# Optimization experiments

Measured on AMD Instinct MI355X. Metric: run time of the kernel, lower is better.

Reference implementation:

```python
import jax, jax.numpy as jnp
import numpy as np

J = 1.0          # coupling constant
PT_PERIOD = 4    # parallel-tempering exchange every PT_PERIOD sweeps


def setup_inputs() -> dict:
    key = jax.random.key(0)
    k1, k2 = jax.random.split(key)
    B, C, L = 32, 16, 256
    # temperatures across the Ising critical region, sorted ascending
    T = jnp.sort(1.5 + 2.0 * jax.random.uniform(k1, (B,), dtype=jnp.float32))
    # spins stored as {0,1} ints; converted to +/-1 inside reference
    spins = jax.random.randint(k2, (B, C, L, L), 0, 2).astype(jnp.int32)
    return {"T": T, "spins": spins, "n_sweeps": 16}


def _neighbor_sum(s):
    # periodic 4-neighbor sum, shape preserved [B,C,L,L]
    return (jnp.roll(s, 1, -1) + jnp.roll(s, -1, -1)
            + jnp.roll(s, 1, -2) + jnp.roll(s, -1, -2))


def _energy(s):
    # total Ising energy per chain: -J * sum_<ij> s_i s_j  -> [B, C]
    return -J * jnp.sum(s * (jnp.roll(s, -1, -1) + jnp.roll(s, -1, -2)), axis=(-1, -2))


def reference(T, spins, n_sweeps):
    B, C, L, _ = spins.shape
    s = spins.astype(jnp.float32) * 2.0 - 1.0          # +/-1 spins
    ii = jnp.arange(L)
    parity = (ii[:, None] + ii[None, :]) % 2            # [L,L] checkerboard
    Tb = T[:, None, None, None]                         # [B,1,1,1]
    beta = 1.0 / T                                      # [B]
    base_key = jax.random.key(42)

    def half_sweep(s, key, color):
        dE = 2.0 * J * s * _neighbor_sum(s)             # local energy change on flip
        u = jax.random.uniform(key, s.shape, dtype=jnp.float32)
        acc = u < jnp.exp(-dE / Tb)                     # Metropolis accept
        mask = (parity == color)                        # update one sub-lattice only
        return jnp.where(mask & acc, -s, s)

    def pt_swap(s, key, pair_parity):
        # attempt swaps between adjacent temperatures (b, b+1) with given pair parity
        E = _energy(s)                                  # [B, C]
        d = (beta[:-1] - beta[1:])[:, None] * (E[:-1] - E[1:])   # [B-1, C]
        u = jax.random.uniform(key, (B - 1, C), dtype=jnp.float32)
        pair_mask = (jnp.arange(B - 1) % 2) == pair_parity
        acc = (u < jnp.exp(d)) & pair_mask[:, None]     # [B-1, C] non-overlapping
        swap_next = jnp.concatenate([acc, jnp.zeros((1, C), bool)], 0)  # swap b<->b+1
        swap_prev = jnp.concatenate([jnp.zeros((1, C), bool), acc], 0)
        s_next = jnp.roll(s, -1, axis=0)
        s_prev = jnp.roll(s, 1, axis=0)
        swn = swap_next[:, :, None, None]
        swp = swap_prev[:, :, None, None]
        return jnp.where(swn, s_next, jnp.where(swp, s_prev, s))

    def sweep(s, t):
        kb = jax.random.fold_in(base_key, t)
        k1, k2, k3 = jax.random.split(kb, 3)
        s = half_sweep(s, k1, 0)   # black sub-lattice
        s = half_sweep(s, k2, 1)   # white sub-lattice
        do_pt = (t % PT_PERIOD) == (PT_PERIOD - 1)
        s = jax.lax.cond(do_pt,
                         lambda s_: pt_swap(s_, k3, (t // PT_PERIOD) % 2),
                         lambda s_: s_, s)
        return s, None

    s, _ = jax.lax.scan(sweep, s, jnp.arange(n_sweeps))
    return s, _energy(s)
```

## Files before the change

kernel.cpp:

```cpp
#include <hip/hip_runtime.h>
#include <stdint.h>


#define BB 32
#define CC 16
#define PLANE 65536
#define NSITE (BB * CC * PLANE)
#define NPAIR ((BB - 1) * CC)

__host__ __device__ __forceinline__ void tf2x32(uint32_t k0, uint32_t k1,
                                                uint32_t c0, uint32_t c1,
                                                uint32_t& o0, uint32_t& o1) {
  uint32_t ks2 = k0 ^ k1 ^ 0x1BD11BDAu;
  uint32_t x0 = c0 + k0;
  uint32_t x1 = c1 + k1;
#define TF_ROT(r) { x0 += x1; x1 = (x1 << (r)) | (x1 >> (32 - (r))); x1 ^= x0; }
  TF_ROT(13) TF_ROT(15) TF_ROT(26) TF_ROT(6)
  x0 += k1;  x1 += ks2 + 1u;
  TF_ROT(17) TF_ROT(29) TF_ROT(16) TF_ROT(24)
  x0 += ks2; x1 += k0 + 2u;
  TF_ROT(13) TF_ROT(15) TF_ROT(26) TF_ROT(6)
  x0 += k0;  x1 += k1 + 3u;
  TF_ROT(17) TF_ROT(29) TF_ROT(16) TF_ROT(24)
  x0 += k1;  x1 += ks2 + 4u;
  TF_ROT(13) TF_ROT(15) TF_ROT(26) TF_ROT(6)
  x0 += ks2; x1 += k0 + 5u;
#undef TF_ROT
  o0 = x0; o1 = x1;
}

__device__ __forceinline__ uint32_t rotl(uint32_t x, int r) {
  return __builtin_amdgcn_alignbit(x, x, 32 - r);
}

__device__ __forceinline__ uint32_t tf_bits(uint32_t k0, uint32_t k1,
                                            uint32_t ks2, uint32_t x1i) {
  uint32_t x0 = k0, x1 = x1i;
#define R4(a,b,c,d) \
  x0 += x1; x1 = rotl(x1, (a)); x1 ^= x0; \
  x0 += x1; x1 = rotl(x1, (b)); x1 ^= x0; \
  x0 += x1; x1 = rotl(x1, (c)); x1 ^= x0; \
  x0 += x1; x1 = rotl(x1, (d)); x1 ^= x0;
  R4(13,15,26,6)  x0 += k1;  x1 += ks2 + 1u;
  R4(17,29,16,24) x0 += ks2; x1 += k0 + 2u;
  R4(13,15,26,6)  x0 += k0;  x1 += k1 + 3u;
  R4(17,29,16,24) x0 += k1;  x1 += ks2 + 4u;
  R4(13,15,26,6)  x0 += ks2; x1 += k0 + 5u;
#undef R4
  return x0 ^ x1;
}

__device__ __forceinline__ float u01(uint32_t bits) {
  return __uint_as_float((bits >> 9) | 0x3f800000u) - 1.0f;
}

__device__ __forceinline__ void mk_thresholds(float tb, uint32_t& M4b,
                                              uint32_t& M8b) {
  float th4 = (float)exp((double)((-4.0f) / tb));
  float th8 = (float)exp((double)((-8.0f) / tb));
  M4b = (uint32_t)ceil((double)th4 * 8388608.0);
  M8b = (uint32_t)ceil((double)th8 * 8388608.0);
}

__device__ __forceinline__ bool pt_accept(int pair, const float* Eplane,
                                          const float* T,
                                          uint32_t k0, uint32_t k1) {
  int b = pair >> 4;
  float d = (1.0f / T[b] - 1.0f / T[b + 1])
          * (Eplane[pair] - Eplane[pair + 16]);
  uint32_t h0, h1;
  tf2x32(k0, k1, 0u, (uint32_t)pair, h0, h1);
  float u = u01(h0 ^ h1);
  float th = (float)exp((double)d);
  return u < th;
}

__device__ __forceinline__ void do_color(uint32_t* __restrict__ tile,
    int w, int lane, int lm, int lp, uint32_t vk, int color,
    uint32_t k0, uint32_t k1, uint32_t ks2, uint32_t M4b, uint32_t M8b) {
#pragma unroll 4
  for (int it = 0; it < 16; ++it) {
    int j  = w + it * 16;
    int rb = j << 6;
    int ju = ((j + 255) & 255) << 6;
    int jd = ((j + 1) & 255) << 6;
    int p  = (j + color) & 1;
    uint32_t soff = (uint32_t)((j << 8) + p);

    uint32_t cur = tile[rb + lane];
    uint32_t up  = tile[ju + lane];
    uint32_t dn  = tile[jd + lane];
    uint32_t pw  = tile[rb + lm];
    uint32_t nw  = tile[rb + lp];
    uint32_t lft = __builtin_amdgcn_alignbit(cur, pw, 24);
    uint32_t rgt = __builtin_amdgcn_alignbit(nw, cur, 8);
    uint32_t kd2 = (up & 0x02020202u) + (dn & 0x02020202u)
                 + (lft & 0x02020202u) + (rgt & 0x02020202u);

    uint32_t flip = 0;
    {
      uint32_t kdi = (kd2 >> (8 * p)) & 0xFFu;
      uint32_t si  = (cur >> (8 * p + 1)) & 1u;
      uint32_t m2  = si ? (8u - kdi) : kdi;
      bool a = true;
      if (m2 < 4u) {
        uint32_t n = tf_bits(k0, k1, ks2, vk + soff) >> 9;
        a = n < (m2 == 2u ? M4b : M8b);
      }
      if (a) flip |= 0xFEu << (8 * p);
    }
    {
      uint32_t kdi = (kd2 >> (8 * p + 16)) & 0xFFu;
      uint32_t si  = (cur >> (8 * p + 17)) & 1u;
      uint32_t m2  = si ? (8u - kdi) : kdi;
      bool a = true;
      if (m2 < 4u) {
        uint32_t n = tf_bits(k0, k1, ks2, vk + soff + 2u) >> 9;
        a = n < (m2 == 2u ? M4b : M8b);
      }
      if (a) flip |= 0xFE0000u << (8 * p);
    }
    tile[rb + lane] = cur ^ flip;
  }
}

__global__ __launch_bounds__(1024) void sweep4_k(
    uint8_t* __restrict__ sg, const int* __restrict__ spins, int doInit,
    const float* __restrict__ T,
    uint4 kS0, uint4 kS1, uint4 kS2, uint4 kS3,
    int tbase, const int* __restrict__ nsw, float* __restrict__ Eplane) {
  __shared__ uint32_t tile[16384];
  int tid = threadIdx.x;
  int bc  = blockIdx.x;
  int b   = bc >> 4;
  uint32_t bcbase = (uint32_t)bc << 16;
  uint32_t* gp = (uint32_t*)(sg + ((size_t)bc << 16));
  uint32_t M4b, M8b;
  mk_thresholds(T[b], M4b, M8b);
  int nswv = *nsw;

  if (doInit) {
    const int4* ip = (const int4*)(spins + ((size_t)bc << 16));
    for (int i = tid; i < 16384; i += 1024) {
      int4 v = ip[i];
      tile[i] = ((uint32_t)(uint8_t)(int8_t)(2 * v.x - 1))
              | ((uint32_t)(uint8_t)(int8_t)(2 * v.y - 1) << 8)
              | ((uint32_t)(uint8_t)(int8_t)(2 * v.z - 1) << 16)
              | ((uint32_t)(uint8_t)(int8_t)(2 * v.w - 1) << 24);
    }
  } else {
    for (int i = tid; i < 4096; i += 1024)
      ((uint4*)tile)[i] = ((const uint4*)gp)[i];
  }
  __syncthreads();

  int w    = __builtin_amdgcn_readfirstlane(tid >> 6);
  int lane = tid & 63;
  int lm   = (lane + 63) & 63, lp = (lane + 1) & 63;

  uint4 keys[4] = {kS0, kS1, kS2, kS3};
#pragma unroll
  for (int ss = 0; ss < 4; ++ss) {
    if (tbase + ss < nswv) {
      uint32_t kA0 = keys[ss].x, kA1 = keys[ss].y;
      uint32_t kB0 = keys[ss].z, kB1 = keys[ss].w;
      uint32_t ksA = kA0 ^ kA1 ^ 0x1BD11BDAu;
      uint32_t ksB = kB0 ^ kB1 ^ 0x1BD11BDAu;
      uint32_t vkA = kA1 + bcbase + (uint32_t)(lane << 2);
      uint32_t vkB = kB1 + bcbase + (uint32_t)(lane << 2);
      do_color(tile, w, lane, lm, lp, vkA, 0, kA0, kA1, ksA, M4b, M8b);
      __syncthreads();
      do_color(tile, w, lane, lm, lp, vkB, 1, kB0, kB1, ksB, M4b, M8b);
      __syncthreads();
    }
  }

  int acc = 0;
  for (int it = 0; it < 16; ++it) {
    int j = w + it * 16;
    uint32_t cur = tile[(j << 6) + lane];
    uint32_t nxt = tile[(j << 6) + lp];
    uint32_t dwn = tile[((((j + 1) & 255)) << 6) + lane];
    uint32_t rsh = (cur >> 8) | (nxt << 24);
    int d = __builtin_popcount((cur ^ rsh) & 0x02020202u)
          + __builtin_popcount((cur ^ dwn) & 0x02020202u);
    acc += 8 - 2 * d;
  }

  for (int i = tid; i < 4096; i += 1024)
    ((uint4*)gp)[i] = ((uint4*)tile)[i];
  __syncthreads();

  for (int off = 32; off > 0; off >>= 1) acc += __shfl_down(acc, off, 64);
  if (lane == 0) tile[w] = (uint32_t)acc;
  __syncthreads();
  if (tid == 0) {
    int tot = 0;
    for (int i = 0; i < 16; ++i) tot += (int)tile[i];
    Eplane[bc] = -(float)tot;
  }
}

__global__ __launch_bounds__(256) void pt_swapD_k(uint8_t* __restrict__ s,
    const float* __restrict__ Eplane, const float* __restrict__ T,
    uint32_t k0, uint32_t k1, int pair_parity, int t,
    const int* __restrict__ nsw) {
  int pc = blockIdx.x;
  int b  = pc >> 4;
  if ((b & 1) != pair_parity) return;
  if (t >= *nsw) return;
  if (!pt_accept(pc, Eplane, T, k0, k1)) return;
  uint4* p0 = (uint4*)(s + ((size_t)pc << 16));
  uint4* p1 = p0 + (CC * PLANE / 16);
  for (int j = threadIdx.x; j < PLANE / 16; j += 256) {
    uint4 a0 = p0[j], a1 = p1[j];
    p0[j] = a1; p1[j] = a0;
  }
}

__device__ __forceinline__ int perm_src(int pc, const float* Eplane,
                                        const float* T, uint32_t k0,
                                        uint32_t k1, int pair_parity,
                                        int t, int nswv) {
  int b = pc >> 4;
  if (t < nswv) {
    if (b < 31 && (b & 1) == pair_parity &&
        pt_accept(pc, Eplane, T, k0, k1)) return pc + 16;
    if (b > 0 && ((b - 1) & 1) == pair_parity &&
        pt_accept(pc - 16, Eplane, T, k0, k1)) return pc - 16;
  }
  return pc;
}

__global__ __launch_bounds__(256) void expand_perm_k(
    const uint8_t* __restrict__ s, float* __restrict__ out,
    const float* __restrict__ Eplane, const float* __restrict__ T,
    uint32_t k0, uint32_t k1, int pair_parity, int t,
    const int* __restrict__ nsw, float* __restrict__ Eout) {
  int pc  = blockIdx.x >> 3;
  int sub = blockIdx.x & 7;
  int src = perm_src(pc, Eplane, T, k0, k1, pair_parity, t, *nsw);
  const uint32_t* p0 = (const uint32_t*)(s + ((size_t)src << 16));
  float4* p1 = (float4*)(out + ((size_t)pc << 14));
  int base = sub * 2048;
  for (int j = threadIdx.x; j < 2048; j += 256) {
    uint32_t v = p0[base + j];
    float4 o;
    o.x = (float)(int8_t)(v);
    o.y = (float)(int8_t)(v >> 8);
    o.z = (float)(int8_t)(v >> 16);
    o.w = (float)(int8_t)(v >> 24);
    p1[base + j] = o;
  }
  if (threadIdx.x == 0 && sub == 0) Eout[pc] = Eplane[src];
}

__global__ void final_eoutD_k(const float* __restrict__ Eplane,
                              const float* __restrict__ T,
                              uint32_t k0, uint32_t k1, int pair_parity,
                              int t, const int* __restrict__ nsw,
                              float* __restrict__ Eout) {
  int pc = threadIdx.x;
  int src = perm_src(pc, Eplane, T, k0, k1, pair_parity, t, *nsw);
  Eout[pc] = Eplane[src];
}

__global__ __launch_bounds__(256) void expand_k(const int8_t* __restrict__ st,
                                                float* __restrict__ out,
                                                int lo, int cnt4) {
  int i = blockIdx.x * 256 + threadIdx.x;
  if (i >= cnt4) return;
  uint32_t v = *(const uint32_t*)(st + lo + 4 * i);
  float4 o;
  o.x = (float)(int8_t)(v);
  o.y = (float)(int8_t)(v >> 8);
  o.z = (float)(int8_t)(v >> 16);
  o.w = (float)(int8_t)(v >> 24);
  ((float4*)out)[(lo >> 2) + i] = o;
}

__global__ __launch_bounds__(256) void expand_head_k(const int8_t* __restrict__ st,
                                                     float* __restrict__ out) {
  uint32_t r[8];
  int t = threadIdx.x;
  for (int u = 0; u < 8; ++u) r[u] = *(const uint32_t*)(st + t * 32 + 4 * u);
  __syncthreads();
  for (int u = 0; u < 8; ++u) {
    uint32_t v = r[u];
    float4 o;
    o.x = (float)(int8_t)(v);
    o.y = (float)(int8_t)(v >> 8);
    o.z = (float)(int8_t)(v >> 16);
    o.w = (float)(int8_t)(v >> 24);
    ((float4*)out)[t * 8 + u] = o;
  }
}

extern "C" void kernel_launch(void* const* d_in, const int* in_sizes, int n_in,
                              void* d_out, int out_size, void* d_ws, size_t ws_size,
                              hipStream_t stream) {
  (void)in_sizes; (void)n_in; (void)out_size;
  const float* T    = (const float*)d_in[0];
  const int*  spins = (const int*)d_in[1];
  const int*  nsw   = (const int*)d_in[2];

  float* outf = (float*)d_out;
  float* Eout = outf + NSITE;

  float*   Eplane = (float*)d_ws;
  uint8_t* wstate = (uint8_t*)d_ws + 4096;
  bool big_ws = (ws_size >= (size_t)NSITE + 4096);
  uint8_t* state = big_ws ? wstate : (uint8_t*)d_out;

  uint32_t k3fa = 0, k3fb = 0;
  for (int g = 0; g < 4; ++g) {
    uint4 kS[4];
    uint32_t k3a = 0, k3b = 0;
    for (int i = 0; i < 4; ++i) {
      int t = 4 * g + i;
      uint32_t kb0, kb1;
      tf2x32(0u, 42u, 0u, (uint32_t)t, kb0, kb1);
      tf2x32(kb0, kb1, 0u, 0u, kS[i].x, kS[i].y);
      tf2x32(kb0, kb1, 0u, 1u, kS[i].z, kS[i].w);
      if (i == 3) tf2x32(kb0, kb1, 0u, 2u, k3a, k3b);
    }
    sweep4_k<<<BB * CC, 1024, 0, stream>>>(state, spins, (g == 0) ? 1 : 0,
                                           T, kS[0], kS[1], kS[2], kS[3],
                                           4 * g, nsw, Eplane);
    if (g < 3) {
      pt_swapD_k<<<NPAIR, 256, 0, stream>>>(state, Eplane, T, k3a, k3b,
                                            g & 1, 4 * g + 3, nsw);
    } else {
      k3fa = k3a; k3fb = k3b;
    }
  }

  if (big_ws) {
    expand_perm_k<<<BB * CC * 8, 256, 0, stream>>>(state, outf, Eplane, T,
                                                   k3fa, k3fb, 1, 15, nsw,
                                                   Eout);
  } else {
    pt_swapD_k<<<NPAIR, 256, 0, stream>>>(state, Eplane, T, k3fa, k3fb,
                                          1, 15, nsw);
    final_eoutD_k<<<1, 512, 0, stream>>>(Eplane, T, k3fa, k3fb, 1, 15,
                                         nsw, Eout);
    for (int lo = NSITE / 4; lo >= 8192; lo >>= 2) {
      int cnt4 = (lo * 3) / 4;
      expand_k<<<(cnt4 + 255) / 256, 256, 0, stream>>>((int8_t*)state, outf,
                                                       lo, cnt4);
    }
    expand_head_k<<<1, 256, 0, stream>>>((int8_t*)state, outf);
  }
}
```

Measured before the change: 1.410 ms.

## Fuse all sweeps and tempering swaps into one persistent kernel with grid barriers

Adds a persistent fused kernel in which each of the 512 blocks keeps its 256x256 lattice plane in shared memory for all 16 sweeps. Blocks meet at software grid barriers built on global atomics, and replica-exchange swaps are done by relabelling a block's logical plane rather than copying data. The int8 state round-trips to global memory between kernels and the separate swap and expand launches go away, and random keys are precomputed at compile time. The old multi-kernel path stays as a fallback behind a completion flag and timeouts, so it adds launch and flag-check overhead. If the 512 blocks of 1024 threads cannot all be resident at once, the barrier times out and that fallback runs.

```diff
diff --git a/kernel.cpp b/kernel.cpp
--- a/kernel.cpp
+++ b/kernel.cpp
@@ -7,6 +7,11 @@
 #define PLANE 65536
 #define NSITE (BB * CC * PLANE)
 #define NPAIR ((BB - 1) * CC)
+#define NBLK (BB * CC)
+
+#define CTL_WORDS 16
+#define REG_TMO  400000ULL
+#define BAR_TMO 1000000ULL
 
 __host__ __device__ __forceinline__ void tf2x32(uint32_t k0, uint32_t k1,
                                                 uint32_t c0, uint32_t c1,
@@ -29,6 +34,47 @@
   o0 = x0; o1 = x1;
 }
 
+constexpr void tf2x32_ce(uint32_t k0, uint32_t k1, uint32_t c0, uint32_t c1,
+                         uint32_t& o0, uint32_t& o1) {
+  uint32_t ks2 = k0 ^ k1 ^ 0x1BD11BDAu;
+  uint32_t x0 = c0 + k0;
+  uint32_t x1 = c1 + k1;
+#define TF_ROT(r) { x0 += x1; x1 = (x1 << (r)) | (x1 >> (32 - (r))); x1 ^= x0; }
+  TF_ROT(13) TF_ROT(15) TF_ROT(26) TF_ROT(6)
+  x0 += k1;  x1 += ks2 + 1u;
+  TF_ROT(17) TF_ROT(29) TF_ROT(16) TF_ROT(24)
+  x0 += ks2; x1 += k0 + 2u;
+  TF_ROT(13) TF_ROT(15) TF_ROT(26) TF_ROT(6)
+  x0 += k0;  x1 += k1 + 3u;
+  TF_ROT(17) TF_ROT(29) TF_ROT(16) TF_ROT(24)
+  x0 += k1;  x1 += ks2 + 4u;
+  TF_ROT(13) TF_ROT(15) TF_ROT(26) TF_ROT(6)
+  x0 += ks2; x1 += k0 + 5u;
+#undef TF_ROT
+  o0 = x0; o1 = x1;
+}
+
+struct KeyTab {
+  uint32_t s[16][4];
+  uint32_t pt[4][2];
+};
+
+constexpr KeyTab make_keys() {
+  KeyTab K{};
+  for (int t = 0; t < 16; ++t) {
+    uint32_t kb0 = 0, kb1 = 0;
+    tf2x32_ce(0u, 42u, 0u, (uint32_t)t, kb0, kb1);
+    tf2x32_ce(kb0, kb1, 0u, 0u, K.s[t][0], K.s[t][1]);
+    tf2x32_ce(kb0, kb1, 0u, 1u, K.s[t][2], K.s[t][3]);
+    if ((t & 3) == 3)
+      tf2x32_ce(kb0, kb1, 0u, 2u, K.pt[t >> 2][0], K.pt[t >> 2][1]);
+  }
+  return K;
+}
+
+constexpr KeyTab HKEYS = make_keys();
+__device__ __constant__ KeyTab DKEYS = make_keys();
+
 __device__ __forceinline__ uint32_t rotl(uint32_t x, int r) {
   return __builtin_amdgcn_alignbit(x, x, 32 - r);
 }
@@ -62,17 +108,23 @@
   M8b = (uint32_t)ceil((double)th8 * 8388608.0);
 }
 
-__device__ __forceinline__ bool pt_accept(int pair, const float* Eplane,
-                                          const float* T,
-                                          uint32_t k0, uint32_t k1) {
-  int b = pair >> 4;
-  float d = (1.0f / T[b] - 1.0f / T[b + 1])
-          * (Eplane[pair] - Eplane[pair + 16]);
+__device__ __forceinline__ bool pt_accept_vals(int pair, float E0, float E1,
+                                               float T0, float T1,
+                                               uint32_t k0, uint32_t k1) {
+  float d = (1.0f / T0 - 1.0f / T1) * (E0 - E1);
   uint32_t h0, h1;
   tf2x32(k0, k1, 0u, (uint32_t)pair, h0, h1);
   float u = u01(h0 ^ h1);
   float th = (float)exp((double)d);
   return u < th;
+}
+
+__device__ __forceinline__ bool pt_accept(int pair, const float* Eplane,
+                                          const float* T,
+                                          uint32_t k0, uint32_t k1) {
+  int b = pair >> 4;
+  return pt_accept_vals(pair, Eplane[pair], Eplane[pair + 16],
+                        T[b], T[b + 1], k0, k1);
 }
 
 __device__ __forceinline__ void do_color(uint32_t* __restrict__ tile,
@@ -124,11 +176,179 @@
   }
 }
 
+__device__ int grid_bar_safe(uint32_t* arrive, uint32_t* depart,
+                             uint32_t* abt, unsigned long long tmo) {
+  __hip_atomic_fetch_add(arrive, 1u, __ATOMIC_ACQ_REL,
+                         __HIP_MEMORY_SCOPE_AGENT);
+  unsigned long long t0 = __builtin_amdgcn_s_memrealtime();
+  for (;;) {
+    if (__hip_atomic_load(abt, __ATOMIC_ACQUIRE, __HIP_MEMORY_SCOPE_AGENT))
+      return 1;
+    if (__hip_atomic_load(arrive, __ATOMIC_ACQUIRE,
+                          __HIP_MEMORY_SCOPE_AGENT) >= (uint32_t)NBLK)
+      break;
+    if (__builtin_amdgcn_s_memrealtime() - t0 > tmo) {
+      __hip_atomic_store(abt, 1u, __ATOMIC_RELEASE, __HIP_MEMORY_SCOPE_AGENT);
+      return 1;
+    }
+    __builtin_amdgcn_s_sleep(8);
+  }
+  uint32_t d = __hip_atomic_fetch_add(depart, 1u, __ATOMIC_ACQ_REL,
+                                      __HIP_MEMORY_SCOPE_AGENT);
+  if (d == (uint32_t)NBLK - 1u) {
+    __hip_atomic_store(arrive, 0u, __ATOMIC_RELAXED,
+                       __HIP_MEMORY_SCOPE_AGENT);
+    __hip_atomic_store(depart, 0u, __ATOMIC_RELAXED,
+                       __HIP_MEMORY_SCOPE_AGENT);
+  }
+  return 0;
+}
+
+__global__ void ctl_init_k(uint32_t* __restrict__ ctl) {
+  if (threadIdx.x < CTL_WORDS) ctl[threadIdx.x] = 0;
+}
+
+__global__ __launch_bounds__(1024) void fused16_k(
+    float* __restrict__ out, const int* __restrict__ spins,
+    const float* __restrict__ T, const int* __restrict__ nsw,
+    float* __restrict__ Ep4 , uint32_t* __restrict__ ctl,
+    float* __restrict__ Eout) {
+  __shared__ uint32_t tile[16384];
+  __shared__ int esc[17];
+
+  int tid = threadIdx.x;
+
+  if (tid == 0)
+    esc[16] = grid_bar_safe(&ctl[0], &ctl[5], &ctl[10], REG_TMO);
+  __syncthreads();
+  if (esc[16]) return;
+  __syncthreads();
+
+  int logical = blockIdx.x;
+
+  {
+    const int4* ip = (const int4*)(spins + ((size_t)logical << 16));
+    for (int i = tid; i < 16384; i += 1024) {
+      int4 v = ip[i];
+      tile[i] = ((uint32_t)(uint8_t)(int8_t)(2 * v.x - 1))
+              | ((uint32_t)(uint8_t)(int8_t)(2 * v.y - 1) << 8)
+              | ((uint32_t)(uint8_t)(int8_t)(2 * v.z - 1) << 16)
+              | ((uint32_t)(uint8_t)(int8_t)(2 * v.w - 1) << 24);
+    }
+  }
+  __syncthreads();
+
+  int w    = __builtin_amdgcn_readfirstlane(tid >> 6);
+  int lane = tid & 63;
+  int lm   = (lane + 63) & 63, lp = (lane + 1) & 63;
+  int nswv = *nsw;
+  int lastTot = 0;
+
+  for (int g = 0; g < 4; ++g) {
+    int b = logical >> 4;
+    uint32_t M4b, M8b;
+    mk_thresholds(T[b], M4b, M8b);
+    uint32_t bcbase = (uint32_t)logical << 16;
+
+#pragma unroll
+    for (int ss = 0; ss < 4; ++ss) {
+      if (4 * g + ss < nswv) {
+        uint32_t kA0 = DKEYS.s[4 * g + ss][0], kA1 = DKEYS.s[4 * g + ss][1];
+        uint32_t kB0 = DKEYS.s[4 * g + ss][2], kB1 = DKEYS.s[4 * g + ss][3];
+        uint32_t ksA = kA0 ^ kA1 ^ 0x1BD11BDAu;
+        uint32_t ksB = kB0 ^ kB1 ^ 0x1BD11BDAu;
+        uint32_t vkA = kA1 + bcbase + (uint32_t)(lane << 2);
+        uint32_t vkB = kB1 + bcbase + (uint32_t)(lane << 2);
+        do_color(tile, w, lane, lm, lp, vkA, 0, kA0, kA1, ksA, M4b, M8b);
+        __syncthreads();
+        do_color(tile, w, lane, lm, lp, vkB, 1, kB0, kB1, ksB, M4b, M8b);
+        __syncthreads();
+      }
+    }
+
+    int acc = 0;
+    for (int it = 0; it < 16; ++it) {
+      int j = w + it * 16;
+      uint32_t cur = tile[(j << 6) + lane];
+      uint32_t nxt = tile[(j << 6) + lp];
+      uint32_t dwn = tile[((((j + 1) & 255)) << 6) + lane];
+      uint32_t rsh = (cur >> 8) | (nxt << 24);
+      int d = __builtin_popcount((cur ^ rsh) & 0x02020202u)
+            + __builtin_popcount((cur ^ dwn) & 0x02020202u);
+      acc += 8 - 2 * d;
+    }
+    for (int off = 32; off > 0; off >>= 1) acc += __shfl_down(acc, off, 64);
+    if (lane == 0) esc[w] = acc;
+    __syncthreads();
+
+    float* Ep = Ep4 + g * NBLK;
+    if (tid == 0) {
+      int tot = 0;
+      for (int i = 0; i < 16; ++i) tot += esc[i];
+      lastTot = tot;
+      __hip_atomic_store(&Ep[logical], -(float)tot, __ATOMIC_RELEASE,
+                         __HIP_MEMORY_SCOPE_AGENT);
+      int st = grid_bar_safe(&ctl[1 + g], &ctl[6 + g], &ctl[10], BAR_TMO);
+      int nl;
+      if (st) {
+        nl = -1;
+      } else {
+        if (g == 3 && blockIdx.x == 0)
+          __hip_atomic_store(&ctl[11], 1u, __ATOMIC_RELEASE,
+                             __HIP_MEMORY_SCOPE_AGENT);
+        nl = logical;
+        int t = 4 * g + 3;
+        if (t < nswv) {
+          int parity = g & 1;
+          if (b < 31 && (b & 1) == parity) {
+            float E0 = __hip_atomic_load(&Ep[logical], __ATOMIC_ACQUIRE,
+                                         __HIP_MEMORY_SCOPE_AGENT);
+            float E1 = __hip_atomic_load(&Ep[logical + 16], __ATOMIC_ACQUIRE,
+                                         __HIP_MEMORY_SCOPE_AGENT);
+            if (pt_accept_vals(logical, E0, E1, T[b], T[b + 1],
+                               DKEYS.pt[g][0], DKEYS.pt[g][1]))
+              nl = logical + 16;
+          } else if (b > 0 && ((b - 1) & 1) == parity) {
+            float E0 = __hip_atomic_load(&Ep[logical - 16], __ATOMIC_ACQUIRE,
+                                         __HIP_MEMORY_SCOPE_AGENT);
+            float E1 = __hip_atomic_load(&Ep[logical], __ATOMIC_ACQUIRE,
+                                         __HIP_MEMORY_SCOPE_AGENT);
+            if (pt_accept_vals(logical - 16, E0, E1, T[b - 1], T[b],
+                               DKEYS.pt[g][0], DKEYS.pt[g][1]))
+              nl = logical - 16;
+          }
+        }
+      }
+      esc[16] = nl;
+    }
+    __syncthreads();
+    int v = esc[16];
+    if (v < 0) return;
+    logical = v;
+    __syncthreads();
+  }
+
+  float4* p1 = ((float4*)out) + ((size_t)logical << 14);
+  for (int i = tid; i < 16384; i += 1024) {
+    uint32_t v = tile[i];
+    float4 o;
+    o.x = (float)(int8_t)(v);
+    o.y = (float)(int8_t)(v >> 8);
+    o.z = (float)(int8_t)(v >> 16);
+    o.w = (float)(int8_t)(v >> 24);
+    p1[i] = o;
+  }
+  if (tid == 0) Eout[logical] = -(float)lastTot;
+}
+
+
 __global__ __launch_bounds__(1024) void sweep4_k(
+    const uint32_t* __restrict__ fok,
     uint8_t* __restrict__ sg, const int* __restrict__ spins, int doInit,
     const float* __restrict__ T,
     uint4 kS0, uint4 kS1, uint4 kS2, uint4 kS3,
     int tbase, const int* __restrict__ nsw, float* __restrict__ Eplane) {
+  if (fok && *fok) return;
   __shared__ uint32_t tile[16384];
   int tid = threadIdx.x;
   int bc  = blockIdx.x;
@@ -201,10 +421,12 @@
   }
 }
 
-__global__ __launch_bounds__(256) void pt_swapD_k(uint8_t* __restrict__ s,
+__global__ __launch_bounds__(256) void pt_swapD_k(
+    const uint32_t* __restrict__ fok, uint8_t* __restrict__ s,
     const float* __restrict__ Eplane, const float* __restrict__ T,
     uint32_t k0, uint32_t k1, int pair_parity, int t,
     const int* __restrict__ nsw) {
+  if (fok && *fok) return;
   int pc = blockIdx.x;
   int b  = pc >> 4;
   if ((b & 1) != pair_parity) return;
@@ -233,15 +455,17 @@
 }
 
 __global__ __launch_bounds__(256) void expand_perm_k(
+    const uint32_t* __restrict__ fok,
     const uint8_t* __restrict__ s, float* __restrict__ out,
     const float* __restrict__ Eplane, const float* __restrict__ T,
     uint32_t k0, uint32_t k1, int pair_parity, int t,
     const int* __restrict__ nsw, float* __restrict__ Eout) {
+  if (fok && *fok) return;
   int pc  = blockIdx.x >> 3;
   int sub = blockIdx.x & 7;
   int src = perm_src(pc, Eplane, T, k0, k1, pair_parity, t, *nsw);
   const uint32_t* p0 = (const uint32_t*)(s + ((size_t)src << 16));
-  float4* p1 = (float4*)(out + ((size_t)pc << 14));
+  float4* p1 = ((float4*)out) + ((size_t)pc << 14);
   int base = sub * 2048;
   for (int j = threadIdx.x; j < 2048; j += 256) {
     uint32_t v = p0[base + j];
@@ -255,19 +479,22 @@
   if (threadIdx.x == 0 && sub == 0) Eout[pc] = Eplane[src];
 }
 
-__global__ void final_eoutD_k(const float* __restrict__ Eplane,
+__global__ void final_eoutD_k(const uint32_t* __restrict__ fok,
+                              const float* __restrict__ Eplane,
                               const float* __restrict__ T,
                               uint32_t k0, uint32_t k1, int pair_parity,
                               int t, const int* __restrict__ nsw,
                               float* __restrict__ Eout) {
+  if (fok && *fok) return;
   int pc = threadIdx.x;
   int src = perm_src(pc, Eplane, T, k0, k1, pair_parity, t, *nsw);
   Eout[pc] = Eplane[src];
 }
 
-__global__ __launch_bounds__(256) void expand_k(const int8_t* __restrict__ st,
-                                                float* __restrict__ out,
-                                                int lo, int cnt4) {
+__global__ __launch_bounds__(256) void expand_k(
+    const uint32_t* __restrict__ fok, const int8_t* __restrict__ st,
+    float* __restrict__ out, int lo, int cnt4) {
+  if (fok && *fok) return;
   int i = blockIdx.x * 256 + threadIdx.x;
   if (i >= cnt4) return;
   uint32_t v = *(const uint32_t*)(st + lo + 4 * i);
@@ -279,8 +506,10 @@
   ((float4*)out)[(lo >> 2) + i] = o;
 }
 
-__global__ __launch_bounds__(256) void expand_head_k(const int8_t* __restrict__ st,
-                                                     float* __restrict__ out) {
+__global__ __launch_bounds__(256) void expand_head_k(
+    const uint32_t* __restrict__ fok, const int8_t* __restrict__ st,
+    float* __restrict__ out) {
+  if (fok && *fok) return;
   uint32_t r[8];
   int t = threadIdx.x;
   for (int u = 0; u < 8; ++u) r[u] = *(const uint32_t*)(st + t * 32 + 4 * u);
@@ -296,6 +525,10 @@
   }
 }
 
+static inline uint4 mk4(const uint32_t k[4]) {
+  uint4 r; r.x = k[0]; r.y = k[1]; r.z = k[2]; r.w = k[3]; return r;
+}
+
 extern "C" void kernel_launch(void* const* d_in, const int* in_sizes, int n_in,
                               void* d_out, int out_size, void* d_ws, size_t ws_size,
                               hipStream_t stream) {
@@ -307,28 +540,32 @@
   float* outf = (float*)d_out;
   float* Eout = outf + NSITE;
 
-  float*   Eplane = (float*)d_ws;
-  uint8_t* wstate = (uint8_t*)d_ws + 4096;
-  bool big_ws = (ws_size >= (size_t)NSITE + 4096);
-  uint8_t* state = big_ws ? wstate : (uint8_t*)d_out;
+  uint8_t* wsb = (uint8_t*)d_ws;
+  bool can_fused = ws_size >= 16384;
+  float*    Ep4 = (float*)wsb;
+  uint32_t* ctl = (uint32_t*)(wsb + 8192);
+  float*    fbE = can_fused ? (float*)(wsb + 12288) : (float*)wsb;
+  const uint32_t* fok = can_fused ? (ctl + 11) : nullptr;
+
+  bool big_ws = ws_size >= (size_t)NSITE + 65536;
+  uint8_t* state = big_ws ? (wsb + 65536) : (uint8_t*)d_out;
+
+  if (can_fused) {
+    ctl_init_k<<<1, 64, 0, stream>>>(ctl);
+    fused16_k<<<NBLK, 1024, 0, stream>>>(outf, spins, T, nsw, Ep4, ctl, Eout);
+  }
 
   uint32_t k3fa = 0, k3fb = 0;
   for (int g = 0; g < 4; ++g) {
-    uint4 kS[4];
-    uint32_t k3a = 0, k3b = 0;
-    for (int i = 0; i < 4; ++i) {
-      int t = 4 * g + i;
-      uint32_t kb0, kb1;
-      tf2x32(0u, 42u, 0u, (uint32_t)t, kb0, kb1);
-      tf2x32(kb0, kb1, 0u, 0u, kS[i].x, kS[i].y);
-      tf2x32(kb0, kb1, 0u, 1u, kS[i].z, kS[i].w);
-      if (i == 3) tf2x32(kb0, kb1, 0u, 2u, k3a, k3b);
-    }
-    sweep4_k<<<BB * CC, 1024, 0, stream>>>(state, spins, (g == 0) ? 1 : 0,
-                                           T, kS[0], kS[1], kS[2], kS[3],
-                                           4 * g, nsw, Eplane);
+    uint32_t k3a = HKEYS.pt[g][0], k3b = HKEYS.pt[g][1];
+    sweep4_k<<<NBLK, 1024, 0, stream>>>(fok, state, spins, (g == 0) ? 1 : 0,
+                                        T, mk4(HKEYS.s[4 * g]),
+                                        mk4(HKEYS.s[4 * g + 1]),
+                                        mk4(HKEYS.s[4 * g + 2]),
+                                        mk4(HKEYS.s[4 * g + 3]),
+                                        4 * g, nsw, fbE);
     if (g < 3) {
-      pt_swapD_k<<<NPAIR, 256, 0, stream>>>(state, Eplane, T, k3a, k3b,
+      pt_swapD_k<<<NPAIR, 256, 0, stream>>>(fok, state, fbE, T, k3a, k3b,
                                             g & 1, 4 * g + 3, nsw);
     } else {
       k3fa = k3a; k3fb = k3b;
@@ -336,19 +573,18 @@
   }
 
   if (big_ws) {
-    expand_perm_k<<<BB * CC * 8, 256, 0, stream>>>(state, outf, Eplane, T,
-                                                   k3fa, k3fb, 1, 15, nsw,
-                                                   Eout);
+    expand_perm_k<<<NBLK * 8, 256, 0, stream>>>(fok, state, outf, fbE, T,
+                                                k3fa, k3fb, 1, 15, nsw, Eout);
   } else {
-    pt_swapD_k<<<NPAIR, 256, 0, stream>>>(state, Eplane, T, k3fa, k3fb,
+    pt_swapD_k<<<NPAIR, 256, 0, stream>>>(fok, state, fbE, T, k3fa, k3fb,
                                           1, 15, nsw);
-    final_eoutD_k<<<1, 512, 0, stream>>>(Eplane, T, k3fa, k3fb, 1, 15,
+    final_eoutD_k<<<1, 512, 0, stream>>>(fok, fbE, T, k3fa, k3fb, 1, 15,
                                          nsw, Eout);
     for (int lo = NSITE / 4; lo >= 8192; lo >>= 2) {
       int cnt4 = (lo * 3) / 4;
-      expand_k<<<(cnt4 + 255) / 256, 256, 0, stream>>>((int8_t*)state, outf,
-                                                       lo, cnt4);
-    }
-    expand_head_k<<<1, 256, 0, stream>>>((int8_t*)state, outf);
-  }
-}
+      expand_k<<<(cnt4 + 255) / 256, 256, 0, stream>>>(fok, (int8_t*)state,
+                                                       outf, lo, cnt4);
+    }
+    expand_head_k<<<1, 256, 0, stream>>>(fok, (int8_t*)state, outf);
+  }
+}
```

Measured after the change: 5.572 ms. 295% more time.
